# Kernel tuning notes

Hardware: AMD Instinct MI355X
Metric: run time of the kernel (lower is better)

## Reference

```python
import jax, jax.numpy as jnp
import numpy as np
import math

L, B, C = 3, 32, 256
HZ, HX, HM = 15, 31, 127
SCALE = 15.0 / 127.0
EPS_BN = 1e-5


def conv2d(x, w, b=None, pad='VALID'):
    y = jax.lax.conv_general_dilated(x, w, (1, 1), pad,
                                     dimension_numbers=('NCHW', 'OIHW', 'NCHW'))
    if b is not None:
        y = y + b[None, :, None, None]
    return y


def conv1x1(x, w, b=None):
    y = jnp.einsum('oc,bchw->bohw', w, x)
    if b is not None:
        y = y + b[None, :, None, None]
    return y


def resize_ac(x, oh, ow):
    # bilinear resize, align_corners=True (matches nn.Upsample(align_corners=True))
    ih, iw = x.shape[-2], x.shape[-1]
    ys = jnp.arange(oh) * ((ih - 1) / (oh - 1))
    xs = jnp.arange(ow) * ((iw - 1) / (ow - 1))
    y0 = jnp.clip(jnp.floor(ys).astype(jnp.int32), 0, ih - 2)
    x0 = jnp.clip(jnp.floor(xs).astype(jnp.int32), 0, iw - 2)
    wy = (ys - y0).astype(x.dtype)
    wx = (xs - x0).astype(x.dtype)
    r = x[..., y0, :] * (1 - wy)[:, None] + x[..., y0 + 1, :] * wy[:, None]
    return r[..., x0] * (1 - wx) + r[..., x0 + 1] * wx


def _hat_int(u):
    # integral of the bilinear hat kernel from -inf to u
    return jnp.where(u <= -1.0, 0.0,
           jnp.where(u <= 0.0, 0.5 * (u + 1.0) ** 2,
           jnp.where(u <= 1.0, 1.0 - 0.5 * (1.0 - u) ** 2, 1.0)))


def _bin_w(lo, hi, n):
    # exact per-grid-point integration weights of PrRoIPool bins, [P, n]
    i = jnp.arange(n, dtype=jnp.float32)
    return _hat_int(hi[:, None] - i) - _hat_int(lo[:, None] - i)


def prroi_pool(feat, boxes, ph=7, pw=7, scale=SCALE):
    # Precise RoI Pooling: exact integral of bilinearly-interpolated feature per bin.
    def one(f, roi):
        x1, y1, x2, y2 = roi * scale
        bh = (y2 - y1) / ph
        bw = (x2 - x1) / pw
        py = jnp.arange(ph, dtype=jnp.float32)
        px = jnp.arange(pw, dtype=jnp.float32)
        Wy = _bin_w(y1 + py * bh, y1 + (py + 1) * bh, f.shape[-2])
        Wx = _bin_w(x1 + px * bw, x1 + (px + 1) * bw, f.shape[-1])
        area = jnp.maximum(bh * bw, 1e-6)
        return jnp.einsum('ph,qw,chw->cpq', Wy, Wx, f) / area
    return jax.vmap(one)(feat, boxes)


def non_local(p, x):
    n, c, h, w = x.shape
    g_x = conv1x1(x, p['nl_g_w'], p['nl_g_b']).reshape(n, -1, h * w).transpose(0, 2, 1)
    th = conv1x1(x, p['nl_th_w'], p['nl_th_b']).reshape(n, -1, h * w).transpose(0, 2, 1)
    ph = conv1x1(x, p['nl_ph_w'], p['nl_ph_b']).reshape(n, -1, h * w)
    pw_ = jax.nn.softmax(jnp.matmul(th, ph), axis=-1) / math.sqrt(c)
    y = jnp.matmul(pw_, g_x).transpose(0, 2, 1).reshape(n, -1, h, w)
    y = conv1x1(y, p['nl_out_w'])  # no bias, then eval-mode BatchNorm
    y = (y - p['bn_m'][None, :, None, None]) / jnp.sqrt(p['bn_v'] + EPS_BN)[None, :, None, None]
    return y * p['bn_g'][None, :, None, None] + p['bn_b'][None, :, None, None]


def chan_z(p, rois):
    b = rois.shape[0]
    th = conv1x1(rois, p['cz_th_w'], p['cz_th_b']).reshape(b, C, -1)
    ph = conv1x1(rois, p['cz_ph_w'], p['cz_ph_b']).reshape(b, C, -1)
    f = jnp.matmul(th, ph.transpose(0, 2, 1))      # [b,C,C] channel Gram
    gw = p['cz_gw'].reshape(C, 2, C)               # grouped conv, out ch = 2g+k
    out = jnp.einsum('gkh,bgh->bgk', gw, f).reshape(b, 2 * C)
    out = jax.nn.relu(out + p['cz_gb'][None])
    out = jnp.einsum('oc,bc->bo', p['cz_aw'], out) + p['cz_ab'][None]
    return out[:, :, None, None]


def mlp_pool(xp, w1, b1, w2, b2):
    return conv1x1(jax.nn.relu(conv1x1(xp, w1, b1)), w2, b2)


def cse_forward(p, zf, xf, mask, box):
    b = zf.shape[0]
    m = jnp.concatenate([mask, 1.0 - mask], axis=1)
    m = jax.nn.relu(conv2d(m, p['ac1_w'], p['ac1_b']))
    m = jax.nn.relu(conv2d(m, p['ac2_w'], p['ac2_b']))
    m = resize_ac(m, HZ - 1, HZ - 1)
    m = conv2d(m, p['ac3_w'], p['ac3_b'], pad='SAME')
    m = resize_ac(m, HZ, HZ)
    m = conv2d(m, p['ac4_w'], p['ac4_b'], pad='SAME')  # [b,1,15,15]

    self_attn = non_local(p, zf)
    rois = prroi_pool(jax.lax.stop_gradient(zf), box)  # zf_raw.detach()
    z_avg = mlp_pool(rois.mean(axis=(2, 3), keepdims=True), p['ap_w1'], p['ap_b1'], p['ap_w2'], p['ap_b2'])
    z_max = mlp_pool(rois.max(axis=(2, 3), keepdims=True), p['mp_w1'], p['mp_b1'], p['mp_w2'], p['mp_b2'])
    z_2n = chan_z(p, rois)
    cues = jnp.concatenate([z_avg, z_max, z_2n], axis=2)  # [b,C,3,1]
    cues = jnp.einsum('ck,bck->bc', p['dr_w'], cues[..., 0]) + p['dr_b'][None]
    cues = jax.nn.sigmoid(cues)[:, :, None, None]

    z_phi = conv1x1(zf, p['phi_w'], p['phi_b']).reshape(b, C, HZ * HZ)
    x_delta = conv1x1(xf, p['delta_w'], p['delta_b']).reshape(b, C, HX * HX).transpose(0, 2, 1)
    sc = jnp.matmul(x_delta, z_phi) / math.sqrt(C)     # [b,961,225]
    mv = m.reshape(b, 1, HZ * HZ).transpose(0, 2, 1)
    sc = jnp.matmul(sc, mv).transpose(0, 2, 1).reshape(b, 1, HX, HX)
    sc = jnp.clip(sc, 0.0, 1.0)

    zf_full = cues * zf + zf + self_attn
    xf_out = cues * xf + xf - sc
    zf_out = zf_full[:, :, 4:11, 4:11]  # size(3)=15 < 20 -> crop
    return zf_out, zf_full, xf_out


PARAM_KEYS = ['nl_g_w', 'nl_g_b', 'nl_th_w', 'nl_th_b', 'nl_ph_w', 'nl_ph_b', 'nl_out_w',
              'bn_g', 'bn_b', 'bn_m', 'bn_v',
              'cz_th_w', 'cz_th_b', 'cz_ph_w', 'cz_ph_b', 'cz_gw', 'cz_gb', 'cz_aw', 'cz_ab',
              'ap_w1', 'ap_b1', 'ap_w2', 'ap_b2', 'mp_w1', 'mp_b1', 'mp_w2', 'mp_b2',
              'dr_w', 'dr_b',
              'ac1_w', 'ac1_b', 'ac2_w', 'ac2_b', 'ac3_w', 'ac3_b', 'ac4_w', 'ac4_b',
              'phi_w', 'phi_b', 'delta_w', 'delta_b']


def setup_inputs() -> dict:
    key = jax.random.key(0)
    ks = iter(jax.random.split(key, 80))
    def rn(shape, s=0.05):
        return jax.random.normal(next(ks), shape, dtype=jnp.float32) * s
    C2 = C // 2
    inp = {
        'zf': rn((L, B, C, HZ, HZ), 1.0),
        'xf': rn((L, B, C, HX, HX), 1.0),
        'mask': jax.random.uniform(next(ks), (B, 1, HM, HM), dtype=jnp.float32),
        'box': jnp.concatenate([
            jax.random.uniform(next(ks), (B, 2), minval=10.0, maxval=40.0),
            jax.random.uniform(next(ks), (B, 2), minval=80.0, maxval=120.0)], axis=1),
        'nl_g_w': rn((L, C2, C)), 'nl_g_b': rn((L, C2)),
        'nl_th_w': rn((L, C2, C)), 'nl_th_b': rn((L, C2)),
        'nl_ph_w': rn((L, C2, C)), 'nl_ph_b': rn((L, C2)),
        'nl_out_w': rn((L, C, C2)),
        'bn_g': 1.0 + rn((L, C)), 'bn_b': rn((L, C)),
        'bn_m': rn((L, C)),
        'bn_v': jax.random.uniform(next(ks), (L, C), minval=0.5, maxval=1.5),
        'cz_th_w': rn((L, C, C)), 'cz_th_b': rn((L, C)),
        'cz_ph_w': rn((L, C, C)), 'cz_ph_b': rn((L, C)),
        'cz_gw': rn((L, 2 * C, C)), 'cz_gb': rn((L, 2 * C)),
        'cz_aw': rn((L, C, 2 * C)), 'cz_ab': rn((L, C)),
        'ap_w1': rn((L, C2, C)), 'ap_b1': rn((L, C2)),
        'ap_w2': rn((L, C, C2)), 'ap_b2': rn((L, C)),
        'mp_w1': rn((L, C2, C)), 'mp_b1': rn((L, C2)),
        'mp_w2': rn((L, C, C2)), 'mp_b2': rn((L, C)),
        'dr_w': rn((L, C, 3)), 'dr_b': rn((L, C)),
        'ac1_w': rn((L, 4, 2, 3, 3)), 'ac1_b': rn((L, 4)),
        'ac2_w': rn((L, 8, 4, 3, 3)), 'ac2_b': rn((L, 8)),
        'ac3_w': rn((L, 4, 8, 3, 3)), 'ac3_b': rn((L, 4)),
        'ac4_w': rn((L, 1, 4, 3, 3)), 'ac4_b': rn((L, 1)),
        'phi_w': rn((L, C, C)), 'phi_b': rn((L, C)),
        'delta_w': rn((L, C, C)), 'delta_b': rn((L, C)),
    }
    return inp


def reference(zf, xf, mask, box,
              nl_g_w, nl_g_b, nl_th_w, nl_th_b, nl_ph_w, nl_ph_b, nl_out_w,
              bn_g, bn_b, bn_m, bn_v,
              cz_th_w, cz_th_b, cz_ph_w, cz_ph_b, cz_gw, cz_gb, cz_aw, cz_ab,
              ap_w1, ap_b1, ap_w2, ap_b2, mp_w1, mp_b1, mp_w2, mp_b2,
              dr_w, dr_b,
              ac1_w, ac1_b, ac2_w, ac2_b, ac3_w, ac3_b, ac4_w, ac4_b,
              phi_w, phi_b, delta_w, delta_b):
    loc = locals()
    p = {k: loc[k] for k in PARAM_KEYS}
    fwd = jax.vmap(cse_forward, in_axes=(0, 0, 0, None, None))
    # returns (zf_out [L,B,C,7,7], zf_raw [L,B,C,15,15], xf_out [L,B,C,31,31])
    return fwd(p, zf, xf, mask, box)
```

## Files before the change

kernel.cpp:

```cpp
#include <hip/hip_runtime.h>
#include <math.h>

#define NL 3
#define NB 32
#define NC 256
#define NC2 128
#define HZ 15
#define ZZ 225
#define XX 961
#define HMD 127

typedef unsigned short u16;
typedef __attribute__((ext_vector_type(8))) unsigned short us8;
typedef __attribute__((ext_vector_type(8))) short bf8v;
typedef __attribute__((ext_vector_type(4))) float f4v;

__device__ __forceinline__ u16 f2bf(float f){
  unsigned int u = __float_as_uint(f);
  unsigned int r = (u + 0x7fffu + ((u>>16)&1u)) >> 16;
  return (u16)r;
}
__device__ __forceinline__ float hat_int(float u){
  if (u <= -1.f) return 0.f;
  if (u <= 0.f){ float t = u + 1.f; return 0.5f*t*t; }
  if (u <= 1.f){ float t = 1.f - u; return 1.f - 0.5f*t*t; }
  return 1.f;
}
__device__ __forceinline__ float dot4(float4 a, float4 b){
  return a.x*b.x + a.y*b.y + a.z*b.z + a.w*b.w;
}
__device__ __forceinline__ float wave_red(float s){
  #pragma unroll
  for (int off=32; off>0; off>>=1) s += __shfl_xor(s, off);
  return s;
}

__global__ __launch_bounds__(256) void k_mask(const float* __restrict__ mask,
    const float* __restrict__ w1, const float* __restrict__ b1,
    const float* __restrict__ w2, const float* __restrict__ b2,
    const float* __restrict__ w3, const float* __restrict__ b3,
    const float* __restrict__ w4, const float* __restrict__ b4,
    float* __restrict__ m3out){
  int lb = blockIdx.x; int l = lb/NB, b = lb%NB;
  int t = threadIdx.x;
  __shared__ float c1s[4][56][56];
  __shared__ float c2s[8][28][28];
  __shared__ float r1s[8][14][14];
  __shared__ float c3s[4][14][14];
  __shared__ float r2s[4][15][15];
  __shared__ int   y0t[14];
  __shared__ float wyt[14];
  __shared__ int   y0t15[15];
  __shared__ float wyt15[15];
  if (t < 14){
    float sy = 122.0f/13.0f;
    float yf = (float)t * sy;
    int y0 = (int)floorf(yf); y0 = min(max(y0,0), 121);
    y0t[t] = y0; wyt[t] = yf - (float)y0;
  } else if (t < 29){
// ... 78 lines not shown
    #pragma unroll
    for (int ic=0; ic<4; ic++)
      #pragma unroll
      for (int ky=-1;ky<=1;ky++){
        int yy = y+ky; if (yy<0||yy>=15) continue;
        #pragma unroll
        for (int kx=-1;kx<=1;kx++){
          int xx = x+kx; if (xx<0||xx>=15) continue;
          acc += wc4[(ic*3+(ky+1))*3+(kx+1)]*r2s[ic][yy][xx];
        }
      }
    m3out[(size_t)lb*ZZ + y*15 + x] = acc;
  }
}

__global__ __launch_bounds__(256) void k_packs(
    const float* __restrict__ thw, const float* __restrict__ thb,
    const float* __restrict__ phw, const float* __restrict__ phb,
    const float* __restrict__ gw,  const float* __restrict__ gb,
    const float* __restrict__ czthw, const float* __restrict__ czthb,
    const float* __restrict__ czphw, const float* __restrict__ czphb,
    const float* __restrict__ outw,
    u16* __restrict__ Wcat, float* __restrict__ bcat,
    u16* __restrict__ Wcz, float* __restrict__ bcz,
    u16* __restrict__ outwb){
  int idx = blockIdx.x*256 + threadIdx.x;
  if (idx < NL*384*256){
    int k = idx & 255; int r = (idx >> 8) % 384; int l = idx/(384*256);
    float v;
    if (r < 128)      v = thw[((size_t)l*128 + r)*256 + k];
    else if (r < 256) v = phw[((size_t)l*128 + (r-128))*256 + k];
    else              v = gw [((size_t)l*128 + (r-256))*256 + k];
    Wcat[idx] = f2bf(v);
  }
  if (idx < NL*512*256){
    int k = idx & 255; int r = (idx >> 8) % 512; int l = idx/(512*256);
    float v;
    if (r < 256) v = czthw[((size_t)l*256 + r)*256 + k];
    else         v = czphw[((size_t)l*256 + (r-256))*256 + k];
    Wcz[idx] = f2bf(v);
  }
  if (idx < NL*NC*NC2) outwb[idx] = f2bf(outw[idx]);
  if (idx < NL*384){
    int r = idx % 384, l = idx/384;
    bcat[idx] = (r<128) ? thb[l*128+r] : (r<256) ? phb[l*128+r-128] : gb[l*128+r-256];
  }
  if (idx < NL*512){
    int r = idx % 512, l = idx/512;
    bcz[idx] = (r<256) ? czthb[l*256+r] : czphb[l*256+r-256];
  }
}

__global__ __launch_bounds__(256) void k_zfall(const float* __restrict__ zf,
    const float* __restrict__ box, const float* __restrict__ m3,
    u16* __restrict__ zfT, float* __restrict__ pavg, float* __restrict__ pmax,
    u16* __restrict__ roisT, float* __restrict__ zm, float* __restrict__ sm){
  int lb = blockIdx.x; int b = lb % NB; int c0 = blockIdx.y*32;
  __shared__ float fld[32*ZZ];
  __shared__ float Wy[7][15], Wx[7][15];
  __shared__ float tmp[32][7][16];
  __shared__ float roi[32][49];
  __shared__ float ms[ZZ];
  __shared__ float area_s;
  int t = threadIdx.x;
// ... 50 lines not shown
  __syncthreads();
  u16* dR = roisT + (size_t)lb*49*NC + c0;
  for (int e=t; e<49*32; e+=256){
    int ci = e & 31, s = e >> 5;
    dR[(size_t)s*NC + ci] = f2bf(roi[ci][s]);
  }
  if (t < 32){
    float s = 0.f, m = -1e30f;
    #pragma unroll
    for (int i=0;i<49;i++){ float v = roi[t][i]; s += v; m = fmaxf(m,v); }
    pavg[(size_t)lb*NC + c0 + t] = s/49.f;
    pmax[(size_t)lb*NC + c0 + t] = m;
  }
}

__global__ __launch_bounds__(256) void k_gxt(const u16* __restrict__ TH3, u16* __restrict__ GXT){
  int lb = blockIdx.x; int z0 = blockIdx.y*32;
  __shared__ u16 lds[32][130];
  int t = threadIdx.x;
  int n = t & 127, zi = t >> 7;
  const u16* src = TH3 + (size_t)lb*ZZ*384 + 256;
  #pragma unroll
  for (int p=0;p<16;p++){
    int z = z0 + zi + p*2;
    lds[zi+p*2][n] = (z < ZZ) ? src[(size_t)z*384 + n] : (u16)0;
  }
  __syncthreads();
  u16* dst = GXT + (size_t)lb*128*256;
  int zi2 = t & 31, ni = t >> 5;
  #pragma unroll
  for (int p=0;p<16;p++){
    int nn = ni + p*8;
    dst[(size_t)nn*256 + z0 + zi2] = lds[zi2][nn];
  }
}

template<bool BPERL, bool HASBIAS, bool OUTBF, bool TROUT>
__global__ __launch_bounds__(256) void k_mg(
    const u16* __restrict__ A0, const u16* __restrict__ B0,
    const float* __restrict__ bias0, void* __restrict__ O0,
    int M, int N, int K, int lda, int ldb, int ldo,
    long Ab, long Bb, long Ob, int ntn)
{
  int lb = blockIdx.y; int l = lb / NB;
  const u16* A = A0 + (size_t)lb*Ab;
  const u16* B = B0 + (BPERL ? (size_t)l : (size_t)lb)*Bb;
  int tm = blockIdx.x / ntn, tn = blockIdx.x % ntn;
  int m0 = tm*64, n0 = tn*64;
  __shared__ u16 Asl[64][40];
  __shared__ u16 Bsl[64][40];
  int t = threadIdx.x;
  int w = t>>6, l6 = t&63;
  int fr = l6&15, kg = (l6>>4)*8;
  int srow = t>>2, sseg = (t&3)*8;
  f4v ac0={0,0,0,0}, ac1={0,0,0,0}, ac2={0,0,0,0}, ac3={0,0,0,0};
  for (int kc=0; kc<K; kc+=32){
    us8 va = {0,0,0,0,0,0,0,0};
    int am = m0 + srow;
    if (am < M) va = *(const us8*)&A[(size_t)am*lda + kc + sseg];
    *(us8*)&Asl[srow][sseg] = va;
    us8 vb = {0,0,0,0,0,0,0,0};
    int bn = n0 + srow;
    if (bn < N) vb = *(const us8*)&B[(size_t)bn*ldb + kc + sseg];
    *(us8*)&Bsl[srow][sseg] = vb;
    __syncthreads();
    bf8v af = *(const bf8v*)&Asl[w*16 + fr][kg];
// ... 21 lines not shown
        u16* out = (u16*)O0 + (size_t)lb*Ob;
        out[(size_t)n*ldo + m] = f2bf((m<M) ? (a[r]+bv) : 0.f);
      } else if (m < M){
        if (OUTBF){
          u16* out = (u16*)O0 + (size_t)lb*Ob;
          out[(size_t)m*ldo + n] = f2bf(a[r]+bv);
        } else {
          float* out = (float*)O0 + (size_t)lb*Ob;
          out[(size_t)m*ldo + n] = a[r]+bv;
        }
      }
    }
  }
}

__global__ __launch_bounds__(256) void k_softmax(const float* __restrict__ S, u16* __restrict__ P){
  int row = blockIdx.x*4 + (threadIdx.x >> 6);
  int lane = threadIdx.x & 63;
  const float* r = S + (size_t)row*ZZ;
  float v[4]; float mx = -1e30f;
  #pragma unroll
  for (int q=0;q<4;q++){
    int j = lane + q*64;
    v[q] = (j<ZZ) ? r[j] : -1e30f;
    mx = fmaxf(mx, v[q]);
  }
  #pragma unroll
  for (int off=32; off>0; off>>=1) mx = fmaxf(mx, __shfl_xor(mx, off));
  float sum = 0.f;
  #pragma unroll
  for (int q=0;q<4;q++){
    v[q] = __expf(v[q]-mx);
    if (lane + q*64 < ZZ) sum += v[q];
  }
  #pragma unroll
  for (int off=32; off>0; off>>=1) sum += __shfl_xor(sum, off);
  float inv = 1.f/(16.f*sum);
  u16* pr = P + (size_t)row*256;
  #pragma unroll
  for (int q=0;q<4;q++){
    int j = lane + q*64;
    pr[j] = (j<ZZ) ? f2bf(v[q]*inv) : (u16)0;
  }
}

__global__ __launch_bounds__(256) void k_outconv_m(const u16* __restrict__ outwb,
    const u16* __restrict__ Ybb,
    const float* __restrict__ bng, const float* __restrict__ bnb,
    const float* __restrict__ bnm, const float* __restrict__ bnv,
    const float* __restrict__ cues, const float* __restrict__ zf,
    float* __restrict__ dzfout, float* __restrict__ dzffull){
  int lb = blockIdx.y; int l = lb/NB;
  const u16* A = outwb + (size_t)l*NC*NC2;
  const u16* B = Ybb + (size_t)lb*ZZ*NC2;
  int tm = blockIdx.x >> 2, tn = blockIdx.x & 3;
  int m0 = tm*64, n0 = tn*64;
  __shared__ u16 Asl[64][40];
  __shared__ u16 Bsl[64][40];
  int t = threadIdx.x;
  int w = t>>6, l6 = t&63;
  int fr = l6&15, kg = (l6>>4)*8;
  int srow = t>>2, sseg = (t&3)*8;
  f4v ac0={0,0,0,0}, ac1={0,0,0,0}, ac2={0,0,0,0}, ac3={0,0,0,0};
  for (int kc=0; kc<NC2; kc+=32){
    us8 va = *(const us8*)&A[(size_t)(m0+srow)*NC2 + kc + sseg];
    *(us8*)&Asl[srow][sseg] = va;
    us8 vb = {0,0,0,0,0,0,0,0};
    int bn = n0 + srow;
    if (bn < ZZ) vb = *(const us8*)&B[(size_t)bn*NC2 + kc + sseg];
    *(us8*)&Bsl[srow][sseg] = vb;
    __syncthreads();
    bf8v af = *(const bf8v*)&Asl[w*16 + fr][kg];
    bf8v b0 = *(const bf8v*)&Bsl[fr][kg];
    bf8v b1 = *(const bf8v*)&Bsl[16+fr][kg];
// ... 15 lines not shown
    #pragma unroll
    for (int r=0;r<4;r++){
      int c = mb + r;
      float scale = bng[l*NC+c] * rsqrtf(bnv[l*NC+c] + 1e-5f);
      float val = (a[r] - bnm[l*NC+c])*scale + bnb[l*NC+c];
      float cu = cues[(size_t)lb*NC + c];
      float zv = zf[((size_t)lb*NC + c)*ZZ + z];
      float rr = cu*zv + zv + val;
      dzffull[((size_t)lb*NC + c)*ZZ + z] = rr;
      if (h>=4 && h<11 && wv2>=4 && wv2<11)
        dzfout[((size_t)lb*NC + c)*49 + (h-4)*7 + (wv2-4)] = rr;
    }
  }
}

__global__ __launch_bounds__(256) void k_mlp1(const float* __restrict__ pavg, const float* __restrict__ pmax,
    const float* __restrict__ aw1, const float* __restrict__ ab1,
    const float* __restrict__ mw1, const float* __restrict__ mb1,
    float* __restrict__ hid){
  int lb = blockIdx.x; int l = lb/NB; int pass = blockIdx.y;
  int t = threadIdx.x, wid = t>>6, lane = t&63;
  int r = blockIdx.z*4 + wid;
  const float* pv = pass ? pmax : pavg;
  const float* w1 = pass ? mw1 : aw1;
  const float* b1 = pass ? mb1 : ab1;
  const float* wr = w1 + (size_t)(l*NC2+r)*NC;
  const float* pr = pv + (size_t)lb*NC;
  float s = dot4(((const float4*)wr)[lane], ((const float4*)pr)[lane]);
  s = wave_red(s);
  if (lane==0) hid[((size_t)lb*2 + pass)*NC2 + r] = fmaxf(s + b1[l*NC2+r], 0.f);
}

__global__ __launch_bounds__(256) void k_mlp2(const float* __restrict__ hid,
    const float* __restrict__ aw2, const float* __restrict__ ab2,
    const float* __restrict__ mw2, const float* __restrict__ mb2,
    float* __restrict__ zavg, float* __restrict__ zmax){
  int lb = blockIdx.x; int l = lb/NB; int pass = blockIdx.y;
  int t = threadIdx.x, wid = t>>6, lane = t&63;
  int c = blockIdx.z*4 + wid;
  const float* w2 = pass ? mw2 : aw2;
  const float* b2 = pass ? mb2 : ab2;
  const float* wr = w2 + (size_t)(l*NC+c)*NC2;
  const float* hr = hid + ((size_t)lb*2 + pass)*NC2;
  float2 wv = ((const float2*)wr)[lane];
  float2 hv = ((const float2*)hr)[lane];
  float s = wave_red(wv.x*hv.x + wv.y*hv.y);
  if (lane==0){
    float* zo = pass ? zmax : zavg;
    zo[(size_t)lb*NC + c] = s + b2[l*NC+c];
  }
}

__global__ __launch_bounds__(256) void k_relw(const float* __restrict__ F,
    const float* __restrict__ gw, const float* __restrict__ gb,
    float* __restrict__ rel){
  int lb = blockIdx.x; int l = lb/NB;
  int t = threadIdx.x, wid = t>>6, lane = t&63;
  int r = blockIdx.y*4 + wid;
  const float* wrow = gw + ((size_t)l*2*NC + r)*NC;
  const float* frow = F + (size_t)lb*NC*NC + (size_t)(r>>1)*NC;
  float s = dot4(((const float4*)wrow)[lane], ((const float4*)frow)[lane]);
  s = wave_red(s);
  if (lane==0) rel[(size_t)lb*2*NC + r] = fmaxf(s + gb[l*2*NC+r], 0.f);
}

__global__ __launch_bounds__(256) void k_z2ncue(const float* __restrict__ rel,
    const float* __restrict__ aw, const float* __restrict__ ab,
    const float* __restrict__ zavg, const float* __restrict__ zmax,
    const float* __restrict__ drw, const float* __restrict__ drb,
    float* __restrict__ cues){
  int lb = blockIdx.x; int l = lb/NB;
  int t = threadIdx.x, wid = t>>6, lane = t&63;
  int c = blockIdx.y*4 + wid;
  const float* arow = aw + ((size_t)l*NC + c)*2*NC;
  const float* rrow = rel + (size_t)lb*2*NC;
  float s = dot4(((const float4*)arow)[lane],    ((const float4*)rrow)[lane])
          + dot4(((const float4*)arow)[lane+64], ((const float4*)rrow)[lane+64]);
  s = wave_red(s);
  if (lane==0){
    float z2 = s + ab[l*NC+c];
    size_t idx = (size_t)lb*NC + c;
    const float* dw = drw + (size_t)(l*NC + c)*3;
    float x = dw[0]*zavg[idx] + dw[1]*zmax[idx] + dw[2]*z2 + drb[l*NC+c];
    cues[idx] = 1.f/(1.f + __expf(-x));
  }
}

__global__ __launch_bounds__(256) void k_zphi(const float* __restrict__ zm, const float* __restrict__ sm,
    const float* __restrict__ phiw, const float* __restrict__ phib, float* __restrict__ zphi){
  int lb = blockIdx.x; int l = lb/NB;
  int t = threadIdx.x, wid = t>>6, lane = t&63;
  int r = blockIdx.y*4 + wid;
  const float* wr = phiw + (size_t)(l*NC + r)*NC;
  const float* zr = zm + (size_t)lb*NC;
  float s = dot4(((const float4*)wr)[lane], ((const float4*)zr)[lane]);
  s = wave_red(s);
  if (lane==0) zphi[(size_t)lb*NC + r] = s + phib[l*NC + r]*sm[lb];
}

__global__ __launch_bounds__(256) void k_wvec(const float* __restrict__ zphi, const float* __restrict__ dw,
    const float* __restrict__ db, float* __restrict__ wvec, float* __restrict__ cb){
  int lb = blockIdx.x; int l = lb/NB;
  __shared__ float zp[NC];
  __shared__ float red[NC];
  int t = threadIdx.x;
  zp[t] = zphi[(size_t)lb*NC + t];
  __syncthreads();
  float s = 0.f;
  const float* dwl = dw + (size_t)l*NC*NC;
  for (int c=0;c<NC;c++) s += zp[c]*dwl[(size_t)c*NC + t];
  wvec[(size_t)lb*NC + t] = s;
  red[t] = zp[t]*db[l*NC + t];
  __syncthreads();
  for (int off2=128; off2>0; off2>>=1){
    if (t < off2) red[t] += red[t+off2];
    __syncthreads();
  }
  if (t==0) cb[lb] = red[0];
}

__global__ __launch_bounds__(256) void k_sc_part(const float* __restrict__ xf,
    const float* __restrict__ wvec, float* __restrict__ part){
  int lb = blockIdx.x, xt = blockIdx.y, cs = blockIdx.z;
  __shared__ float wv[64];
  int t = threadIdx.x;
  if (t < 64) wv[t] = wvec[(size_t)lb*NC + cs*64 + t];
  __syncthreads();
  int x = xt*256 + t;
  if (x >= XX) return;
  const float* xb = xf + ((size_t)lb*NC + cs*64)*XX + x;
  float s = 0.f;
  #pragma unroll 8
  for (int c=0;c<64;c++) s += wv[c]*xb[(size_t)c*XX];
  part[((size_t)lb*4 + cs)*XX + x] = s;
}

__global__ __launch_bounds__(256) void k_xfout2(const float* __restrict__ xf,
    const float* __restrict__ part, const float* __restrict__ cb,
    const float* __restrict__ cues, float* __restrict__ out){
  int bc = blockIdx.y;
  int x = blockIdx.x*256 + threadIdx.x;
  if (x >= XX) return;
  int lb = bc >> 8;
  const float* pp = part + (size_t)lb*4*XX + x;
  float scv = pp[0] + pp[XX] + pp[2*XX] + pp[3*XX];
  scv = fminf(fmaxf((scv + cb[lb])*0.0625f, 0.f), 1.f);
  float cu = cues[bc];
  out[(size_t)bc*XX + x] = (1.f+cu)*xf[(size_t)bc*XX + x] - scv;
}

extern "C" void kernel_launch(void* const* d_in, const int* in_sizes, int n_in,
                              void* d_out, int out_size, void* d_ws, size_t ws_size,
                              hipStream_t stream){
  const float* zf      = (const float*)d_in[0];
  const float* xf      = (const float*)d_in[1];
  const float* maskp   = (const float*)d_in[2];
  const float* box     = (const float*)d_in[3];
  const float* nl_g_w  = (const float*)d_in[4];
  const float* nl_g_b  = (const float*)d_in[5];
  const float* nl_th_w = (const float*)d_in[6];
  const float* nl_th_b = (const float*)d_in[7];
  const float* nl_ph_w = (const float*)d_in[8];
  const float* nl_ph_b = (const float*)d_in[9];
// ... 27 lines not shown
  const float* ac3_w   = (const float*)d_in[37];
  const float* ac3_b   = (const float*)d_in[38];
  const float* ac4_w   = (const float*)d_in[39];
  const float* ac4_b   = (const float*)d_in[40];
  const float* phi_w   = (const float*)d_in[41];
  const float* phi_b   = (const float*)d_in[42];
  const float* delta_w = (const float*)d_in[43];
  const float* delta_b = (const float*)d_in[44];
  (void)in_sizes; (void)n_in; (void)out_size; (void)ws_size;

  float* ws = (float*)d_ws;
  size_t off = 0;
  auto alloc = [&](size_t n){ size_t o = off; off += (n + 15) & ~(size_t)15; return o; };
  float* TH3f  = ws + alloc((size_t)NL*NB*ZZ*384/2);
  float* Sb    = ws + alloc((size_t)NL*NB*ZZ*ZZ);
  u16* TH3  = (u16*)TH3f;
  float* Freg  = TH3f;
  float* zfTf  = ws + alloc((size_t)NL*NB*ZZ*NC/2);
  float* Pbf   = ws + alloc((size_t)NL*NB*ZZ*256/2);
  float* GXTf  = ws + alloc((size_t)NL*NB*128*256/2);
  float* Ybbf  = ws + alloc((size_t)NL*NB*ZZ*NC2/2);
  float* CZ3Tf = ws + alloc((size_t)NL*NB*512*64/2);
  float* roisTf= ws + alloc((size_t)NL*NB*49*NC/2);
  float* Wcatf = ws + alloc((size_t)NL*384*256/2);
  float* Wczf  = ws + alloc((size_t)NL*512*256/2);
  float* outwbf= ws + alloc((size_t)NL*NC*NC2/2);
  u16 *zfT=(u16*)zfTf, *Pb=(u16*)Pbf, *GXT=(u16*)GXTf, *Ybb=(u16*)Ybbf,
      *CZ3T=(u16*)CZ3Tf, *roisT=(u16*)roisTf, *Wcat=(u16*)Wcatf,
      *Wcz=(u16*)Wczf, *outwb=(u16*)outwbf;
  float* bcat = ws + alloc((size_t)NL*384);
  float* bcz  = ws + alloc((size_t)NL*512);
  float* m3   = ws + alloc((size_t)NL*NB*ZZ);
  float* pavg = ws + alloc((size_t)NL*NB*NC);
  float* pmax = ws + alloc((size_t)NL*NB*NC);
  float* zavg = ws + alloc((size_t)NL*NB*NC);
  float* zmax = ws + alloc((size_t)NL*NB*NC);
  float* cues = ws + alloc((size_t)NL*NB*NC);
  float* zm   = ws + alloc((size_t)NL*NB*NC);
  float* zphi = ws + alloc((size_t)NL*NB*NC);
  float* wvec = ws + alloc((size_t)NL*NB*NC);
  float* sm   = ws + alloc((size_t)NL*NB);
  float* cbuf = ws + alloc((size_t)NL*NB);
  float* part = ws + alloc((size_t)NL*NB*4*XX);
  float* hidb = ws + alloc((size_t)NL*NB*2*NC2);
  float* relb = ws + alloc((size_t)NL*NB*2*NC);

  float* outp    = (float*)d_out;
  float* o_zfout = outp;
  float* o_zffull= outp + (size_t)NL*NB*NC*49;
  float* o_xfout = o_zffull + (size_t)NL*NB*NC*ZZ;

  k_mask<<<NL*NB, 256, 0, stream>>>(maskp, ac1_w, ac1_b, ac2_w, ac2_b,
                                     ac3_w, ac3_b, ac4_w, ac4_b, m3);
  k_packs<<<(NL*512*256+255)/256, 256, 0, stream>>>(
      nl_th_w, nl_th_b, nl_ph_w, nl_ph_b, nl_g_w, nl_g_b,
      cz_th_w, cz_th_b, cz_ph_w, cz_ph_b, nl_out_w,
      Wcat, bcat, Wcz, bcz, outwb);
  k_zfall<<<dim3(NL*NB, 8), 256, 0, stream>>>(zf, box, m3, zfT, pavg, pmax,
                                               roisT, zm, sm);

  k_mg<true,true,true,false><<<dim3(24, NL*NB), 256, 0, stream>>>(
      zfT, Wcat, bcat, TH3, ZZ, 384, NC, 256, 256, 384,
      (long)ZZ*256, (long)384*256, (long)ZZ*384, 6);
  k_mg<false,false,false,false><<<dim3(16, NL*NB), 256, 0, stream>>>(
      TH3, TH3+128, nullptr, Sb, ZZ, ZZ, NC2, 384, 384, ZZ,
      (long)ZZ*384, (long)ZZ*384, (long)ZZ*ZZ, 4);
  k_softmax<<<(NL*NB*ZZ)/4, 256, 0, stream>>>(Sb, Pb);
  k_gxt<<<dim3(NL*NB, 8), 256, 0, stream>>>(TH3, GXT);
  k_mg<false,false,true,false><<<dim3(8, NL*NB), 256, 0, stream>>>(
      Pb, GXT, nullptr, Ybb, ZZ, NC2, 256, 256, 256, NC2,
      (long)ZZ*256, (long)128*256, (long)ZZ*NC2, 2);

  k_mlp1<<<dim3(NL*NB, 2, 32), 256, 0, stream>>>(pavg, pmax, ap_w1, ap_b1, mp_w1, mp_b1, hidb);
  k_mlp2<<<dim3(NL*NB, 2, 64), 256, 0, stream>>>(hidb, ap_w2, ap_b2, mp_w2, mp_b2, zavg, zmax);
  k_mg<true,true,true,true><<<dim3(8, NL*NB), 256, 0, stream>>>(
      roisT, Wcz, bcz, CZ3T, 49, 512, NC, 256, 256, 64,
      (long)49*256, (long)512*256, (long)512*64, 8);
  k_mg<false,false,false,false><<<dim3(16, NL*NB), 256, 0, stream>>>(
      CZ3T, CZ3T+256*64, nullptr, Freg, NC, NC, 64, 64, 64, NC,
      (long)512*64, (long)512*64, (long)NC*NC, 4);
  k_relw<<<dim3(NL*NB, 128), 256, 0, stream>>>(Freg, cz_gw, cz_gb, relb);
  k_z2ncue<<<dim3(NL*NB, 64), 256, 0, stream>>>(relb, cz_aw, cz_ab,
                                                 zavg, zmax, dr_w, dr_b, cues);

  k_outconv_m<<<dim3(16, NL*NB), 256, 0, stream>>>(outwb, Ybb, bn_g, bn_b, bn_m, bn_v,
                                                    cues, zf, o_zfout, o_zffull);

  k_zphi<<<dim3(NL*NB, 64), 256, 0, stream>>>(zm, sm, phi_w, phi_b, zphi);
  k_wvec<<<NL*NB, 256, 0, stream>>>(zphi, delta_w, delta_b, wvec, cbuf);
  k_sc_part<<<dim3(NL*NB, 4, 4), 256, 0, stream>>>(xf, wvec, part);
  k_xfout2<<<dim3(4, NL*NB*NC), 256, 0, stream>>>(xf, part, cbuf, cues, o_xfout);
}
```

Baseline: 312.8 us.

## Merge independent kernels into six multi-role launches by dependency level

Groups the many small kernels of the pipeline into six 'super-kernels' (sk_a..sk_f). Each one dispatches on blockIdx ranges to run the independent stages of the same dependency level, such as the QKV GEMM alongside the MLP and zphi GEMV, or the attention scores alongside gxt, mlp2, the F GEMM and wvec. The aim is to cut launch count and fill the GPU with concurrent independent work instead of many under-occupied small launches. In exchange, each block reserves the largest shared-memory footprint of any branch, which may lower occupancy. The F buffer also gets its own workspace allocation instead of aliasing TH3, since both are now live at the same time.

```diff
diff --git a/kernel.cpp b/kernel.cpp
--- a/kernel.cpp
+++ b/kernel.cpp
@@ -35,14 +35,13 @@
   return s;
 }
 
-__global__ __launch_bounds__(256) void k_mask(const float* __restrict__ mask,
+__device__ void d_mask(int lb, int t, const float* __restrict__ mask,
     const float* __restrict__ w1, const float* __restrict__ b1,
     const float* __restrict__ w2, const float* __restrict__ b2,
     const float* __restrict__ w3, const float* __restrict__ b3,
     const float* __restrict__ w4, const float* __restrict__ b4,
     float* __restrict__ m3out){
-  int lb = blockIdx.x; int l = lb/NB, b = lb%NB;
-  int t = threadIdx.x;
+  int l = lb/NB, b = lb%NB;
   __shared__ float c1s[4][56][56];
   __shared__ float c2s[8][28][28];
   __shared__ float r1s[8][14][14];
@@ -151,7 +150,7 @@
   }
 }
 
-__global__ __launch_bounds__(256) void k_packs(
+__device__ void d_packs(int idx,
     const float* __restrict__ thw, const float* __restrict__ thb,
     const float* __restrict__ phw, const float* __restrict__ phb,
     const float* __restrict__ gw,  const float* __restrict__ gb,
@@ -161,7 +160,6 @@
     u16* __restrict__ Wcat, float* __restrict__ bcat,
     u16* __restrict__ Wcz, float* __restrict__ bcz,
     u16* __restrict__ outwb){
-  int idx = blockIdx.x*256 + threadIdx.x;
   if (idx < NL*384*256){
     int k = idx & 255; int r = (idx >> 8) % 384; int l = idx/(384*256);
     float v;
@@ -185,6 +183,23 @@
   if (idx < NL*512){
     int r = idx % 512, l = idx/512;
     bcz[idx] = (r<256) ? czthb[l*256+r] : czphb[l*256+r-256];
+  }
+}
+
+__global__ __launch_bounds__(256) void sk_a(const float* __restrict__ mask,
+    const float* w1, const float* b1, const float* w2, const float* b2,
+    const float* w3, const float* b3, const float* w4, const float* b4,
+    float* m3out,
+    const float* thw, const float* thb, const float* phw, const float* phb,
+    const float* gw, const float* gb,
+    const float* czthw, const float* czthb, const float* czphw, const float* czphb,
+    const float* outw, u16* Wcat, float* bcat, u16* Wcz, float* bcz, u16* outwb){
+  int bid = blockIdx.x, t = threadIdx.x;
+  if (bid < NL*NB){
+    d_mask(bid, t, mask, w1, b1, w2, b2, w3, b3, w4, b4, m3out);
+  } else {
+    d_packs((bid - NL*NB)*256 + t, thw, thb, phw, phb, gw, gb,
+            czthw, czthb, czphw, czphb, outw, Wcat, bcat, Wcz, bcz, outwb);
   }
 }
 
@@ -265,42 +280,20 @@
   }
 }
 
-__global__ __launch_bounds__(256) void k_gxt(const u16* __restrict__ TH3, u16* __restrict__ GXT){
-  int lb = blockIdx.x; int z0 = blockIdx.y*32;
-  __shared__ u16 lds[32][130];
-  int t = threadIdx.x;
-  int n = t & 127, zi = t >> 7;
-  const u16* src = TH3 + (size_t)lb*ZZ*384 + 256;
-  #pragma unroll
-  for (int p=0;p<16;p++){
-    int z = z0 + zi + p*2;
-    lds[zi+p*2][n] = (z < ZZ) ? src[(size_t)z*384 + n] : (u16)0;
-  }
-  __syncthreads();
-  u16* dst = GXT + (size_t)lb*128*256;
-  int zi2 = t & 31, ni = t >> 5;
-  #pragma unroll
-  for (int p=0;p<16;p++){
-    int nn = ni + p*8;
-    dst[(size_t)nn*256 + z0 + zi2] = lds[zi2][nn];
-  }
-}
-
 template<bool BPERL, bool HASBIAS, bool OUTBF, bool TROUT>
-__global__ __launch_bounds__(256) void k_mg(
+__device__ void d_mg(int bid, int t,
     const u16* __restrict__ A0, const u16* __restrict__ B0,
     const float* __restrict__ bias0, void* __restrict__ O0,
     int M, int N, int K, int lda, int ldb, int ldo,
-    long Ab, long Bb, long Ob, int ntn)
+    long Ab, long Bb, long Ob, int ntn, int ntiles)
 {
-  int lb = blockIdx.y; int l = lb / NB;
+  int lb = bid / ntiles; int tile = bid % ntiles; int l = lb / NB;
   const u16* A = A0 + (size_t)lb*Ab;
   const u16* B = B0 + (BPERL ? (size_t)l : (size_t)lb)*Bb;
-  int tm = blockIdx.x / ntn, tn = blockIdx.x % ntn;
+  int tm = tile / ntn, tn = tile % ntn;
   int m0 = tm*64, n0 = tn*64;
   __shared__ u16 Asl[64][40];
   __shared__ u16 Bsl[64][40];
-  int t = threadIdx.x;
   int w = t>>6, l6 = t&63;
   int fr = l6&15, kg = (l6>>4)*8;
   int srow = t>>2, sseg = (t&3)*8;
@@ -352,9 +345,160 @@
   }
 }
 
-__global__ __launch_bounds__(256) void k_softmax(const float* __restrict__ S, u16* __restrict__ P){
-  int row = blockIdx.x*4 + (threadIdx.x >> 6);
-  int lane = threadIdx.x & 63;
+__device__ void d_mlp1(int bid, int t, const float* __restrict__ pavg, const float* __restrict__ pmax,
+    const float* __restrict__ aw1, const float* __restrict__ ab1,
+    const float* __restrict__ mw1, const float* __restrict__ mb1,
+    float* __restrict__ hid){
+  int lb = bid >> 6; int rem = bid & 63; int pass = rem >> 5; int zb = rem & 31;
+  int l = lb/NB;
+  int wid = t>>6, lane = t&63;
+  int r = zb*4 + wid;
+  const float* pv = pass ? pmax : pavg;
+  const float* w1 = pass ? mw1 : aw1;
+  const float* b1 = pass ? mb1 : ab1;
+  const float* wr = w1 + (size_t)(l*NC2+r)*NC;
+  const float* pr = pv + (size_t)lb*NC;
+  float s = dot4(((const float4*)wr)[lane], ((const float4*)pr)[lane]);
+  s = wave_red(s);
+  if (lane==0) hid[((size_t)lb*2 + pass)*NC2 + r] = fmaxf(s + b1[l*NC2+r], 0.f);
+}
+
+__device__ void d_zphi(int bid, int t, const float* __restrict__ zm, const float* __restrict__ sm,
+    const float* __restrict__ phiw, const float* __restrict__ phib, float* __restrict__ zphi){
+  int lb = bid >> 6; int rb = bid & 63; int l = lb/NB;
+  int wid = t>>6, lane = t&63;
+  int r = rb*4 + wid;
+  const float* wr = phiw + (size_t)(l*NC + r)*NC;
+  const float* zr = zm + (size_t)lb*NC;
+  float s = dot4(((const float4*)wr)[lane], ((const float4*)zr)[lane]);
+  s = wave_red(s);
+  if (lane==0) zphi[(size_t)lb*NC + r] = s + phib[l*NC + r]*sm[lb];
+}
+
+__global__ __launch_bounds__(256) void sk_b(
+    const u16* zfT, const u16* Wcat, const float* bcat, u16* TH3,
+    const float* pavg, const float* pmax,
+    const float* ap_w1, const float* ap_b1, const float* mp_w1, const float* mp_b1, float* hidb,
+    const u16* roisT, const u16* Wcz, const float* bcz, u16* CZ3T,
+    const float* zm, const float* sm, const float* phi_w, const float* phi_b, float* zphi){
+  int bid = blockIdx.x, t = threadIdx.x;
+  const int N1 = 96*24, N2 = N1 + 96*64, N3 = N2 + 96*8;
+  if (bid < N1){
+    d_mg<true,true,true,false>(bid, t, zfT, Wcat, bcat, TH3, ZZ, 384, NC, 256, 256, 384,
+        (long)ZZ*256, (long)384*256, (long)ZZ*384, 6, 24);
+  } else if (bid < N2){
+    d_mlp1(bid - N1, t, pavg, pmax, ap_w1, ap_b1, mp_w1, mp_b1, hidb);
+  } else if (bid < N3){
+    d_mg<true,true,true,true>(bid - N2, t, roisT, Wcz, bcz, CZ3T, 49, 512, NC, 256, 256, 64,
+        (long)49*256, (long)512*256, (long)512*64, 8, 8);
+  } else {
+    d_zphi(bid - N3, t, zm, sm, phi_w, phi_b, zphi);
+  }
+}
+
+__device__ void d_gxt(int bid, int t, const u16* __restrict__ TH3, u16* __restrict__ GXT){
+  int lb = bid >> 3; int z0 = (bid & 7)*32;
+  __shared__ u16 lds[32][130];
+  int n = t & 127, zi = t >> 7;
+  const u16* src = TH3 + (size_t)lb*ZZ*384 + 256;
+  #pragma unroll
+  for (int p=0;p<16;p++){
+    int z = z0 + zi + p*2;
+    lds[zi+p*2][n] = (z < ZZ) ? src[(size_t)z*384 + n] : (u16)0;
+  }
+  __syncthreads();
+  u16* dst = GXT + (size_t)lb*128*256;
+  int zi2 = t & 31, ni = t >> 5;
+  #pragma unroll
+  for (int p=0;p<16;p++){
+    int nn = ni + p*8;
+    dst[(size_t)nn*256 + z0 + zi2] = lds[zi2][nn];
+  }
+}
+
+__device__ void d_mlp2(int bid, int t, const float* __restrict__ hid,
+    const float* __restrict__ aw2, const float* __restrict__ ab2,
+    const float* __restrict__ mw2, const float* __restrict__ mb2,
+    float* __restrict__ zavg, float* __restrict__ zmax){
+  int lb = bid >> 7; int rem = bid & 127; int pass = rem >> 6; int cb = rem & 63;
+  int l = lb/NB;
+  int wid = t>>6, lane = t&63;
+  int c = cb*4 + wid;
+  const float* w2 = pass ? mw2 : aw2;
+  const float* b2 = pass ? mb2 : ab2;
+  const float* wr = w2 + (size_t)(l*NC+c)*NC2;
+  const float* hr = hid + ((size_t)lb*2 + pass)*NC2;
+  float2 wv = ((const float2*)wr)[lane];
+  float2 hv = ((const float2*)hr)[lane];
+  float s = wave_red(wv.x*hv.x + wv.y*hv.y);
+  if (lane==0){
+    float* zo = pass ? zmax : zavg;
+    zo[(size_t)lb*NC + c] = s + b2[l*NC+c];
+  }
+}
+
+__device__ void d_wvec(int lb, int t, const float* __restrict__ zphi, const float* __restrict__ dw,
+    const float* __restrict__ db, float* __restrict__ wvec, float* __restrict__ cb){
+  int l = lb/NB;
+  __shared__ float zp[NC];
+  __shared__ float red[NC];
+  zp[t] = zphi[(size_t)lb*NC + t];
+  __syncthreads();
+  float s = 0.f;
+  const float* dwl = dw + (size_t)l*NC*NC;
+  for (int c=0;c<NC;c++) s += zp[c]*dwl[(size_t)c*NC + t];
+  wvec[(size_t)lb*NC + t] = s;
+  red[t] = zp[t]*db[l*NC + t];
+  __syncthreads();
+  for (int off2=128; off2>0; off2>>=1){
+    if (t < off2) red[t] += red[t+off2];
+    __syncthreads();
+  }
+  if (t==0) cb[lb] = red[0];
+}
+
+__global__ __launch_bounds__(256) void sk_c(
+    const u16* TH3, float* Sb,
+    u16* GXT,
+    const float* hidb, const float* ap_w2, const float* ap_b2,
+    const float* mp_w2, const float* mp_b2, float* zavg, float* zmax,
+    const u16* CZ3T, float* Fbuf,
+    const float* zphi, const float* delta_w, const float* delta_b, float* wvec, float* cbuf){
+  int bid = blockIdx.x, t = threadIdx.x;
+  const int N1 = 96*16, N2 = N1 + 96*8, N3 = N2 + 96*128, N4 = N3 + 96*16;
+  if (bid < N1){
+    d_mg<false,false,false,false>(bid, t, TH3, TH3+128, nullptr, Sb, ZZ, ZZ, NC2, 384, 384, ZZ,
+        (long)ZZ*384, (long)ZZ*384, (long)ZZ*ZZ, 4, 16);
+  } else if (bid < N2){
+    d_gxt(bid - N1, t, TH3, GXT);
+  } else if (bid < N3){
+    d_mlp2(bid - N2, t, hidb, ap_w2, ap_b2, mp_w2, mp_b2, zavg, zmax);
+  } else if (bid < N4){
+    d_mg<false,false,false,false>(bid - N3, t, CZ3T, CZ3T+256*64, nullptr, Fbuf, NC, NC, 64, 64, 64, NC,
+        (long)512*64, (long)512*64, (long)NC*NC, 4, 16);
+  } else {
+    d_wvec(bid - N4, t, zphi, delta_w, delta_b, wvec, cbuf);
+  }
+}
+
+__device__ void d_sc_part(int bid, int t, const float* __restrict__ xf,
+    const float* __restrict__ wvec, float* __restrict__ part){
+  int lb = bid >> 4; int rem = bid & 15; int xt = rem >> 2, cs = rem & 3;
+  __shared__ float wv[64];
+  if (t < 64) wv[t] = wvec[(size_t)lb*NC + cs*64 + t];
+  __syncthreads();
+  int x = xt*256 + t;
+  if (x >= XX) return;
+  const float* xb = xf + ((size_t)lb*NC + cs*64)*XX + x;
+  float s = 0.f;
+  #pragma unroll 8
+  for (int c=0;c<64;c++) s += wv[c]*xb[(size_t)c*XX];
+  part[((size_t)lb*4 + cs)*XX + x] = s;
+}
+
+__device__ void d_softmax(int bid, int t, const float* __restrict__ S, u16* __restrict__ P){
+  int row = bid*4 + (t >> 6);
+  int lane = t & 63;
   const float* r = S + (size_t)row*ZZ;
   float v[4]; float mx = -1e30f;
   #pragma unroll
@@ -382,20 +526,83 @@
   }
 }
 
-__global__ __launch_bounds__(256) void k_outconv_m(const u16* __restrict__ outwb,
+__device__ void d_relw(int bid, int t, const float* __restrict__ F,
+    const float* __restrict__ gw, const float* __restrict__ gb,
+    float* __restrict__ rel){
+  int lb = bid >> 7; int rb = bid & 127; int l = lb/NB;
+  int wid = t>>6, lane = t&63;
+  int r = rb*4 + wid;
+  const float* wrow = gw + ((size_t)l*2*NC + r)*NC;
+  const float* frow = F + (size_t)lb*NC*NC + (size_t)(r>>1)*NC;
+  float s = dot4(((const float4*)wrow)[lane], ((const float4*)frow)[lane]);
+  s = wave_red(s);
+  if (lane==0) rel[(size_t)lb*2*NC + r] = fmaxf(s + gb[l*2*NC+r], 0.f);
+}
+
+__global__ __launch_bounds__(256) void sk_d(
+    const float* xf, const float* wvec, float* part,
+    const float* Sb, u16* Pb,
+    const float* Fbuf, const float* cz_gw, const float* cz_gb, float* relb){
+  int bid = blockIdx.x, t = threadIdx.x;
+  const int N1 = 96*16, N2 = N1 + 5400;
+  if (bid < N1){
+    d_sc_part(bid, t, xf, wvec, part);
+  } else if (bid < N2){
+    d_softmax(bid - N1, t, Sb, Pb);
+  } else {
+    d_relw(bid - N2, t, Fbuf, cz_gw, cz_gb, relb);
+  }
+}
+
+__device__ void d_z2ncue(int bid, int t, const float* __restrict__ rel,
+    const float* __restrict__ aw, const float* __restrict__ ab,
+    const float* __restrict__ zavg, const float* __restrict__ zmax,
+    const float* __restrict__ drw, const float* __restrict__ drb,
+    float* __restrict__ cues){
+  int lb = bid >> 6; int cb = bid & 63; int l = lb/NB;
+  int wid = t>>6, lane = t&63;
+  int c = cb*4 + wid;
+  const float* arow = aw + ((size_t)l*NC + c)*2*NC;
+  const float* rrow = rel + (size_t)lb*2*NC;
+  float s = dot4(((const float4*)arow)[lane],    ((const float4*)rrow)[lane])
+          + dot4(((const float4*)arow)[lane+64], ((const float4*)rrow)[lane+64]);
+  s = wave_red(s);
+  if (lane==0){
+    float z2 = s + ab[l*NC+c];
+    size_t idx = (size_t)lb*NC + c;
+    const float* dw = drw + (size_t)(l*NC + c)*3;
+    float x = dw[0]*zavg[idx] + dw[1]*zmax[idx] + dw[2]*z2 + drb[l*NC+c];
+    cues[idx] = 1.f/(1.f + __expf(-x));
+  }
+}
+
+__global__ __launch_bounds__(256) void sk_e(
+    const u16* Pb, const u16* GXT, u16* Ybb,
+    const float* relb, const float* cz_aw, const float* cz_ab,
+    const float* zavg, const float* zmax, const float* dr_w, const float* dr_b, float* cues){
+  int bid = blockIdx.x, t = threadIdx.x;
+  const int N1 = 96*8;
+  if (bid < N1){
+    d_mg<false,false,true,false>(bid, t, Pb, GXT, nullptr, Ybb, ZZ, NC2, 256, 256, 256, NC2,
+        (long)ZZ*256, (long)128*256, (long)ZZ*NC2, 2, 8);
+  } else {
+    d_z2ncue(bid - N1, t, relb, cz_aw, cz_ab, zavg, zmax, dr_w, dr_b, cues);
+  }
+}
+
+__device__ void d_outconv(int bid, int t, const u16* __restrict__ outwb,
     const u16* __restrict__ Ybb,
     const float* __restrict__ bng, const float* __restrict__ bnb,
     const float* __restrict__ bnm, const float* __restrict__ bnv,
     const float* __restrict__ cues, const float* __restrict__ zf,
     float* __restrict__ dzfout, float* __restrict__ dzffull){
-  int lb = blockIdx.y; int l = lb/NB;
+  int lb = bid >> 4; int tile = bid & 15; int l = lb/NB;
   const u16* A = outwb + (size_t)l*NC*NC2;
   const u16* B = Ybb + (size_t)lb*ZZ*NC2;
-  int tm = blockIdx.x >> 2, tn = blockIdx.x & 3;
+  int tm = tile >> 2, tn = tile & 3;
   int m0 = tm*64, n0 = tn*64;
   __shared__ u16 Asl[64][40];
   __shared__ u16 Bsl[64][40];
-  int t = threadIdx.x;
   int w = t>>6, l6 = t&63;
   int fr = l6&15, kg = (l6>>4)*8;
   int srow = t>>2, sseg = (t&3)*8;
@@ -441,132 +648,11 @@
   }
 }
 
-__global__ __launch_bounds__(256) void k_mlp1(const float* __restrict__ pavg, const float* __restrict__ pmax,
-    const float* __restrict__ aw1, const float* __restrict__ ab1,
-    const float* __restrict__ mw1, const float* __restrict__ mb1,
-    float* __restrict__ hid){
-  int lb = blockIdx.x; int l = lb/NB; int pass = blockIdx.y;
-  int t = threadIdx.x, wid = t>>6, lane = t&63;
-  int r = blockIdx.z*4 + wid;
-  const float* pv = pass ? pmax : pavg;
-  const float* w1 = pass ? mw1 : aw1;
-  const float* b1 = pass ? mb1 : ab1;
-  const float* wr = w1 + (size_t)(l*NC2+r)*NC;
-  const float* pr = pv + (size_t)lb*NC;
-  float s = dot4(((const float4*)wr)[lane], ((const float4*)pr)[lane]);
-  s = wave_red(s);
-  if (lane==0) hid[((size_t)lb*2 + pass)*NC2 + r] = fmaxf(s + b1[l*NC2+r], 0.f);
-}
-
-__global__ __launch_bounds__(256) void k_mlp2(const float* __restrict__ hid,
-    const float* __restrict__ aw2, const float* __restrict__ ab2,
-    const float* __restrict__ mw2, const float* __restrict__ mb2,
-    float* __restrict__ zavg, float* __restrict__ zmax){
-  int lb = blockIdx.x; int l = lb/NB; int pass = blockIdx.y;
-  int t = threadIdx.x, wid = t>>6, lane = t&63;
-  int c = blockIdx.z*4 + wid;
-  const float* w2 = pass ? mw2 : aw2;
-  const float* b2 = pass ? mb2 : ab2;
-  const float* wr = w2 + (size_t)(l*NC+c)*NC2;
-  const float* hr = hid + ((size_t)lb*2 + pass)*NC2;
-  float2 wv = ((const float2*)wr)[lane];
-  float2 hv = ((const float2*)hr)[lane];
-  float s = wave_red(wv.x*hv.x + wv.y*hv.y);
-  if (lane==0){
-    float* zo = pass ? zmax : zavg;
-    zo[(size_t)lb*NC + c] = s + b2[l*NC+c];
-  }
-}
-
-__global__ __launch_bounds__(256) void k_relw(const float* __restrict__ F,
-    const float* __restrict__ gw, const float* __restrict__ gb,
-    float* __restrict__ rel){
-  int lb = blockIdx.x; int l = lb/NB;
-  int t = threadIdx.x, wid = t>>6, lane = t&63;
-  int r = blockIdx.y*4 + wid;
-  const float* wrow = gw + ((size_t)l*2*NC + r)*NC;
-  const float* frow = F + (size_t)lb*NC*NC + (size_t)(r>>1)*NC;
-  float s = dot4(((const float4*)wrow)[lane], ((const float4*)frow)[lane]);
-  s = wave_red(s);
-  if (lane==0) rel[(size_t)lb*2*NC + r] = fmaxf(s + gb[l*2*NC+r], 0.f);
-}
-
-__global__ __launch_bounds__(256) void k_z2ncue(const float* __restrict__ rel,
-    const float* __restrict__ aw, const float* __restrict__ ab,
-    const float* __restrict__ zavg, const float* __restrict__ zmax,
-    const float* __restrict__ drw, const float* __restrict__ drb,
-    float* __restrict__ cues){
-  int lb = blockIdx.x; int l = lb/NB;
-  int t = threadIdx.x, wid = t>>6, lane = t&63;
-  int c = blockIdx.y*4 + wid;
-  const float* arow = aw + ((size_t)l*NC + c)*2*NC;
-  const float* rrow = rel + (size_t)lb*2*NC;
-  float s = dot4(((const float4*)arow)[lane],    ((const float4*)rrow)[lane])
-          + dot4(((const float4*)arow)[lane+64], ((const float4*)rrow)[lane+64]);
-  s = wave_red(s);
-  if (lane==0){
-    float z2 = s + ab[l*NC+c];
-    size_t idx = (size_t)lb*NC + c;
-    const float* dw = drw + (size_t)(l*NC + c)*3;
-    float x = dw[0]*zavg[idx] + dw[1]*zmax[idx] + dw[2]*z2 + drb[l*NC+c];
-    cues[idx] = 1.f/(1.f + __expf(-x));
-  }
-}
-
-__global__ __launch_bounds__(256) void k_zphi(const float* __restrict__ zm, const float* __restrict__ sm,
-    const float* __restrict__ phiw, const float* __restrict__ phib, float* __restrict__ zphi){
-  int lb = blockIdx.x; int l = lb/NB;
-  int t = threadIdx.x, wid = t>>6, lane = t&63;
-  int r = blockIdx.y*4 + wid;
-  const float* wr = phiw + (size_t)(l*NC + r)*NC;
-  const float* zr = zm + (size_t)lb*NC;
-  float s = dot4(((const float4*)wr)[lane], ((const float4*)zr)[lane]);
-  s = wave_red(s);
-  if (lane==0) zphi[(size_t)lb*NC + r] = s + phib[l*NC + r]*sm[lb];
-}
-
-__global__ __launch_bounds__(256) void k_wvec(const float* __restrict__ zphi, const float* __restrict__ dw,
-    const float* __restrict__ db, float* __restrict__ wvec, float* __restrict__ cb){
-  int lb = blockIdx.x; int l = lb/NB;
-  __shared__ float zp[NC];
-  __shared__ float red[NC];
-  int t = threadIdx.x;
-  zp[t] = zphi[(size_t)lb*NC + t];
-  __syncthreads();
-  float s = 0.f;
-  const float* dwl = dw + (size_t)l*NC*NC;
-  for (int c=0;c<NC;c++) s += zp[c]*dwl[(size_t)c*NC + t];
-  wvec[(size_t)lb*NC + t] = s;
-  red[t] = zp[t]*db[l*NC + t];
-  __syncthreads();
-  for (int off2=128; off2>0; off2>>=1){
-    if (t < off2) red[t] += red[t+off2];
-    __syncthreads();
-  }
-  if (t==0) cb[lb] = red[0];
-}
-
-__global__ __launch_bounds__(256) void k_sc_part(const float* __restrict__ xf,
-    const float* __restrict__ wvec, float* __restrict__ part){
-  int lb = blockIdx.x, xt = blockIdx.y, cs = blockIdx.z;
-  __shared__ float wv[64];
-  int t = threadIdx.x;
-  if (t < 64) wv[t] = wvec[(size_t)lb*NC + cs*64 + t];
-  __syncthreads();
-  int x = xt*256 + t;
-  if (x >= XX) return;
-  const float* xb = xf + ((size_t)lb*NC + cs*64)*XX + x;
-  float s = 0.f;
-  #pragma unroll 8
-  for (int c=0;c<64;c++) s += wv[c]*xb[(size_t)c*XX];
-  part[((size_t)lb*4 + cs)*XX + x] = s;
-}
-
-__global__ __launch_bounds__(256) void k_xfout2(const float* __restrict__ xf,
+__device__ void d_xfout(int bid, int t, const float* __restrict__ xf,
     const float* __restrict__ part, const float* __restrict__ cb,
     const float* __restrict__ cues, float* __restrict__ out){
-  int bc = blockIdx.y;
-  int x = blockIdx.x*256 + threadIdx.x;
+  int bc = bid >> 2; int xt = bid & 3;
+  int x = xt*256 + t;
   if (x >= XX) return;
   int lb = bc >> 8;
   const float* pp = part + (size_t)lb*4*XX + x;
@@ -574,6 +660,20 @@
   scv = fminf(fmaxf((scv + cb[lb])*0.0625f, 0.f), 1.f);
   float cu = cues[bc];
   out[(size_t)bc*XX + x] = (1.f+cu)*xf[(size_t)bc*XX + x] - scv;
+}
+
+__global__ __launch_bounds__(256) void sk_f(
+    const u16* outwb, const u16* Ybb,
+    const float* bn_g, const float* bn_b, const float* bn_m, const float* bn_v,
+    const float* cues, const float* zf, float* o_zfout, float* o_zffull,
+    const float* xf, const float* part, const float* cbuf, float* o_xfout){
+  int bid = blockIdx.x, t = threadIdx.x;
+  const int N1 = 96*16;
+  if (bid < N1){
+    d_outconv(bid, t, outwb, Ybb, bn_g, bn_b, bn_m, bn_v, cues, zf, o_zfout, o_zffull);
+  } else {
+    d_xfout(bid - N1, t, xf, part, cbuf, cues, o_xfout);
+  }
 }
 
 extern "C" void kernel_launch(void* const* d_in, const int* in_sizes, int n_in,
@@ -631,8 +731,7 @@
   auto alloc = [&](size_t n){ size_t o = off; off += (n + 15) & ~(size_t)15; return o; };
   float* TH3f  = ws + alloc((size_t)NL*NB*ZZ*384/2);
   float* Sb    = ws + alloc((size_t)NL*NB*ZZ*ZZ);
-  u16* TH3  = (u16*)TH3f;
-  float* Freg  = TH3f;
+  float* Fbuf  = ws + alloc((size_t)NL*NB*NC*NC);
   float* zfTf  = ws + alloc((size_t)NL*NB*ZZ*NC/2);
   float* Pbf   = ws + alloc((size_t)NL*NB*ZZ*256/2);
   float* GXTf  = ws + alloc((size_t)NL*NB*128*256/2);
@@ -642,6 +741,7 @@
   float* Wcatf = ws + alloc((size_t)NL*384*256/2);
   float* Wczf  = ws + alloc((size_t)NL*512*256/2);
   float* outwbf= ws + alloc((size_t)NL*NC*NC2/2);
+  u16* TH3  = (u16*)TH3f;
   u16 *zfT=(u16*)zfTf, *Pb=(u16*)Pbf, *GXT=(u16*)GXTf, *Ybb=(u16*)Ybbf,
       *CZ3T=(u16*)CZ3Tf, *roisT=(u16*)roisTf, *Wcat=(u16*)Wcatf,
       *Wcz=(u16*)Wczf, *outwb=(u16*)outwbf;
@@ -667,44 +767,24 @@
   float* o_zffull= outp + (size_t)NL*NB*NC*49;
   float* o_xfout = o_zffull + (size_t)NL*NB*NC*ZZ;
 
-  k_mask<<<NL*NB, 256, 0, stream>>>(maskp, ac1_w, ac1_b, ac2_w, ac2_b,
-                                     ac3_w, ac3_b, ac4_w, ac4_b, m3);
-  k_packs<<<(NL*512*256+255)/256, 256, 0, stream>>>(
+  sk_a<<<NL*NB + (NL*512*256+255)/256, 256, 0, stream>>>(
+      maskp, ac1_w, ac1_b, ac2_w, ac2_b, ac3_w, ac3_b, ac4_w, ac4_b, m3,
       nl_th_w, nl_th_b, nl_ph_w, nl_ph_b, nl_g_w, nl_g_b,
       cz_th_w, cz_th_b, cz_ph_w, cz_ph_b, nl_out_w,
       Wcat, bcat, Wcz, bcz, outwb);
   k_zfall<<<dim3(NL*NB, 8), 256, 0, stream>>>(zf, box, m3, zfT, pavg, pmax,
                                                roisT, zm, sm);
-
-  k_mg<true,true,true,false><<<dim3(24, NL*NB), 256, 0, stream>>>(
-      zfT, Wcat, bcat, TH3, ZZ, 384, NC, 256, 256, 384,
-      (long)ZZ*256, (long)384*256, (long)ZZ*384, 6);
-  k_mg<false,false,false,false><<<dim3(16, NL*NB), 256, 0, stream>>>(
-      TH3, TH3+128, nullptr, Sb, ZZ, ZZ, NC2, 384, 384, ZZ,
-      (long)ZZ*384, (long)ZZ*384, (long)ZZ*ZZ, 4);
-  k_softmax<<<(NL*NB*ZZ)/4, 256, 0, stream>>>(Sb, Pb);
-  k_gxt<<<dim3(NL*NB, 8), 256, 0, stream>>>(TH3, GXT);
-  k_mg<false,false,true,false><<<dim3(8, NL*NB), 256, 0, stream>>>(
-      Pb, GXT, nullptr, Ybb, ZZ, NC2, 256, 256, 256, NC2,
-      (long)ZZ*256, (long)128*256, (long)ZZ*NC2, 2);
-
-  k_mlp1<<<dim3(NL*NB, 2, 32), 256, 0, stream>>>(pavg, pmax, ap_w1, ap_b1, mp_w1, mp_b1, hidb);
-  k_mlp2<<<dim3(NL*NB, 2, 64), 256, 0, stream>>>(hidb, ap_w2, ap_b2, mp_w2, mp_b2, zavg, zmax);
-  k_mg<true,true,true,true><<<dim3(8, NL*NB), 256, 0, stream>>>(
-      roisT, Wcz, bcz, CZ3T, 49, 512, NC, 256, 256, 64,
-      (long)49*256, (long)512*256, (long)512*64, 8);
-  k_mg<false,false,false,false><<<dim3(16, NL*NB), 256, 0, stream>>>(
-      CZ3T, CZ3T+256*64, nullptr, Freg, NC, NC, 64, 64, 64, NC,
-      (long)512*64, (long)512*64, (long)NC*NC, 4);
-  k_relw<<<dim3(NL*NB, 128), 256, 0, stream>>>(Freg, cz_gw, cz_gb, relb);
-  k_z2ncue<<<dim3(NL*NB, 64), 256, 0, stream>>>(relb, cz_aw, cz_ab,
-                                                 zavg, zmax, dr_w, dr_b, cues);
-
-  k_outconv_m<<<dim3(16, NL*NB), 256, 0, stream>>>(outwb, Ybb, bn_g, bn_b, bn_m, bn_v,
-                                                    cues, zf, o_zfout, o_zffull);
-
-  k_zphi<<<dim3(NL*NB, 64), 256, 0, stream>>>(zm, sm, phi_w, phi_b, zphi);
-  k_wvec<<<NL*NB, 256, 0, stream>>>(zphi, delta_w, delta_b, wvec, cbuf);
-  k_sc_part<<<dim3(NL*NB, 4, 4), 256, 0, stream>>>(xf, wvec, part);
-  k_xfout2<<<dim3(4, NL*NB*NC), 256, 0, stream>>>(xf, part, cbuf, cues, o_xfout);
-}
+  sk_b<<<96*24 + 96*64 + 96*8 + 96*64, 256, 0, stream>>>(
+      zfT, Wcat, bcat, TH3, pavg, pmax, ap_w1, ap_b1, mp_w1, mp_b1, hidb,
+      roisT, Wcz, bcz, CZ3T, zm, sm, phi_w, phi_b, zphi);
+  sk_c<<<96*16 + 96*8 + 96*128 + 96*16 + 96, 256, 0, stream>>>(
+      TH3, Sb, GXT, hidb, ap_w2, ap_b2, mp_w2, mp_b2, zavg, zmax,
+      CZ3T, Fbuf, zphi, delta_w, delta_b, wvec, cbuf);
+  sk_d<<<96*16 + 5400 + 96*128, 256, 0, stream>>>(
+      xf, wvec, part, Sb, Pb, Fbuf, cz_gw, cz_gb, relb);
+  sk_e<<<96*8 + 96*64, 256, 0, stream>>>(
+      Pb, GXT, Ybb, relb, cz_aw, cz_ab, zavg, zmax, dr_w, dr_b, cues);
+  sk_f<<<96*16 + 4*NL*NB*NC, 256, 0, stream>>>(
+      outwb, Ybb, bn_g, bn_b, bn_m, bn_v, cues, zf, o_zfout, o_zffull,
+      xf, part, cbuf, o_xfout);
+}
```

New measurement: 281.3 us. 10.1% less time.
